# Kernel tuning notes

Measured on AMD Instinct MI355X. Metric: run time of the kernel, lower is better.

Reference implementation:

```python
import jax, jax.numpy as jnp
import numpy as np

B, S, D = 32, 512, 1024
H, HD = 16, 64          # num_heads, head_dim
K = 64                  # downsampling_k
NEG = -9e15             # -9000000000000000.0 in source


def setup_inputs() -> dict:
    key0 = jax.random.key(0)
    ks = jax.random.split(key0, 8)
    glorot = lambda k, shape, fan: jax.random.uniform(k, shape, jnp.float32,
                                                      -np.sqrt(6.0 / fan), np.sqrt(6.0 / fan))
    fan = D + H * HD  # glorot_uniform over (hidden, heads*head_dim)
    return {
        "query": jax.random.normal(ks[0], (B, S, D), jnp.float32),
        "key": jax.random.normal(ks[1], (B, S, D), jnp.float32),
        "value": jax.random.normal(ks[2], (B, S, D), jnp.float32),
        "query_kernel": glorot(ks[3], (D, H, HD), fan),
        "key_kernel": glorot(ks[4], (D, H, HD), fan),
        "value_kernel": glorot(ks[5], (D, H, HD), fan),
        "key_downsample_mat": (1.0 / K) * jax.random.normal(ks[6], (K, S), jnp.float32),
        "value_downsample_mat": (1.0 / K) * jax.random.normal(ks[7], (K, S), jnp.float32),
    }


def reference(query, key, value, query_kernel, key_kernel, value_kernel,
              key_downsample_mat, value_downsample_mat):
    # Linformer-style downsampling of K/V along the sequence axis: [B,S,D] -> [B,K,D]
    key_ds = jnp.einsum('ks,bsd->bkd', key_downsample_mat, key)
    val_ds = jnp.einsum('ks,bsd->bkd', value_downsample_mat, value)

    # Per-head projections
    q = jnp.einsum('bsd,dnh->bsnh', query, query_kernel)   # [B,S,H,HD]
    k = jnp.einsum('bkd,dnh->bknh', key_ds, key_kernel)    # [B,K,H,HD]
    v = jnp.einsum('bkd,dnh->bknh', val_ds, value_kernel)  # [B,K,H,HD]

    # Masked softmax attention over the downsampled key set
    scores = jnp.einsum('bqnh,bknh->bnqk', q, k)           # [B,H,S,K]
    # Source builds tril over [S, K_down] then slices first K cols (no-op here)
    mask = jnp.tril(jnp.ones((S, K), dtype=bool))          # [S,K], broadcasts over B,H
    scores = jnp.where(mask, scores, NEG)
    attn = jax.nn.softmax(scores, axis=-1)                 # dropout deterministic (train=False)

    a_v = jnp.einsum('bnqk,bknh->bqnh', attn, v)           # [B,S,H,HD]
    return a_v.reshape(B, S, H * HD)
```

## Files before the change

kernel.cpp:

```cpp
#include <hip/hip_runtime.h>
#include <stdint.h>

#define B_   32
#define S_   512
#define D_   1024
#define H_   16
#define HD_  64
#define KD_  64
#define NH_  1024

typedef __attribute__((ext_vector_type(8))) short short8;
typedef __attribute__((ext_vector_type(4))) float floatx4;

#define GAS __attribute__((address_space(1)))
#define LAS __attribute__((address_space(3)))

__device__ __forceinline__ ushort f2bf(float f) {
  uint32_t u = __float_as_uint(f);
  u = u + 0x7FFFu + ((u >> 16) & 1u);
  return (ushort)(u >> 16);
}

__device__ __forceinline__ float bf2f(ushort h) {
  return __uint_as_float(((uint32_t)h) << 16);
}

__device__ __forceinline__ void gload_lds16(const void* g, void* l) {
  __builtin_amdgcn_global_load_lds((const GAS uint32_t*)g, (LAS uint32_t*)l, 16, 0, 0);
}

#define BARRIER() asm volatile("s_barrier" ::: "memory")
#define WAITLGKM() asm volatile("s_waitcnt lgkmcnt(0)" ::: "memory")

__global__ __launch_bounds__(256) void cvt_split(const float* __restrict__ kdm,
                                                 const float* __restrict__ vdm,
                                                 ushort* __restrict__ hi,
                                                 ushort* __restrict__ lo) {
  int i = blockIdx.x * 256 + threadIdx.x;
  const float* src = (i < 8192) ? kdm : vdm;
  int j = i & 8191;
  float4 v = ((const float4*)src)[j];
  ushort4 h, l;
  h.x = f2bf(v.x); l.x = f2bf(v.x - bf2f(h.x));
  h.y = f2bf(v.y); l.y = f2bf(v.y - bf2f(h.y));
  h.z = f2bf(v.z); l.z = f2bf(v.z - bf2f(h.z));
  h.w = f2bf(v.w); l.w = f2bf(v.w - bf2f(h.w));
  ((ushort4*)hi)[i] = h;
  ((ushort4*)lo)[i] = l;
}

__global__ __launch_bounds__(256, 6) void fused_pre(
    const float* __restrict__ query, const float* __restrict__ key,
    const float* __restrict__ value, const float* __restrict__ qk,
    const float* __restrict__ kkm, const float* __restrict__ vkm,
    const ushort* __restrict__ dsm_hi, const ushort* __restrict__ dsm_lo,
    ushort* __restrict__ q_bf, ushort* __restrict__ qkT,
    ushort* __restrict__ kkT, ushort* __restrict__ vkT,
    ushort* __restrict__ outk, ushort* __restrict__ outv) {
  __shared__ __align__(16) char smem[26624];
  const int blk = blockIdx.x;
  const int tid = threadIdx.x;

  if (blk < 512) {
    const int bz = (blk & 7) + ((blk >> 6) << 3);
    const int t  = (blk >> 3) & 7;
    const int z = bz >> 5, b = bz & 31;
    const int c0 = t * 128;
    const float* in = z ? value : key;
    ushort* out     = z ? outv : outk;
    const ushort* Ah = dsm_hi + (size_t)z * (KD_ * S_);
    const ushort* Al = dsm_lo + (size_t)z * (KD_ * S_);

    ushort* lAh = (ushort*)smem;
    ushort* lAl = (ushort*)(smem + 4096);
    uint*   lBh = (uint*)(smem + 8192);
    uint*   lBl = (uint*)(smem + 17408);

    const int lane = tid & 63, w = tid >> 6;
    const int lr = lane & 15, lg = lane >> 4;
    const int wn = w * 32;
    const int lam = tid & 31;
    const int d0 = lam * 4;
    const int sp = tid >> 5;

    floatx4 acc[4][2];
#pragma unroll
    for (int m = 0; m < 4; ++m)
#pragma unroll
      for (int n = 0; n < 2; ++n) acc[m][n] = (floatx4){0.f, 0.f, 0.f, 0.f};

    for (int k0 = 0; k0 < S_; k0 += 32) {
      {
        size_t src = (size_t)(tid >> 2) * S_ + k0 + (size_t)(tid & 3) * 8;
        gload_lds16(Ah + src, lAh + w * 512);
        gload_lds16(Al + src, lAl + w * 512);
      }
      float4 ra[2], rb[2];
#pragma unroll
      for (int si = 0; si < 2; ++si) {
        int s = sp * 2 + si * 16;
        const float* p = in + ((size_t)(b * S_ + k0 + s)) * D_ + c0 + d0;
        ra[si] = *(const float4*)p;
        rb[si] = *(const float4*)(p + D_);
      }
      const int swz = lam & 12;
#pragma unroll
      for (int si = 0; si < 2; ++si) {
        int col = (sp + si * 8) ^ swz;
        const float* pa = (const float*)&ra[si];
        const float* pb = (const float*)&rb[si];
#pragma unroll
        for (int i = 0; i < 4; ++i) {
          ushort h0 = f2bf(pa[i]);
          ushort l0 = f2bf(pa[i] - bf2f(h0));
          ushort h1 = f2bf(pb[i]);
          ushort l1 = f2bf(pb[i] - bf2f(h1));
          lBh[(d0 + i) * 18 + col] = (uint)h0 | ((uint)h1 << 16);
          lBl[(d0 + i) * 18 + col] = (uint)l0 | ((uint)l1 << 16);
        }
      }
      __syncthreads();
      short8 bh[2], bl[2];
#pragma unroll
      for (int n = 0; n < 2; ++n) {
        int d = wn + n * 16 + lr;
        int off = d * 18 + ((lg * 4) ^ ((d >> 2) & 12));
        bh[n] = *(const short8*)&lBh[off];
        bl[n] = *(const short8*)&lBl[off];
      }
#pragma unroll
      for (int m = 0; m < 4; ++m) {
        int aoff = (m * 16 + lr) * 32 + lg * 8;
        short8 ah = *(const short8*)&lAh[aoff];
        short8 al = *(const short8*)&lAl[aoff];
#pragma unroll
        for (int n = 0; n < 2; ++n) {
          acc[m][n] = __builtin_amdgcn_mfma_f32_16x16x32_bf16(ah, bh[n], acc[m][n], 0, 0, 0);
          acc[m][n] = __builtin_amdgcn_mfma_f32_16x16x32_bf16(ah, bl[n], acc[m][n], 0, 0, 0);
          acc[m][n] = __builtin_amdgcn_mfma_f32_16x16x32_bf16(al, bh[n], acc[m][n], 0, 0, 0);
        }
      }
      __syncthreads();
    }
    size_t obase = (size_t)b * KD_ * D_;
#pragma unroll
    for (int m = 0; m < 4; ++m)
#pragma unroll
      for (int n = 0; n < 2; ++n)
#pragma unroll
        for (int r = 0; r < 4; ++r)
          out[obase + (size_t)(m * 16 + lg * 4 + r) * D_ + c0 + wn + n * 16 + lr] =
              f2bf(acc[m][n][r]);

  } else if (blk < 512 + 3072) {
    const int blk2 = blk - 512;
    const int tz = blk2 >> 10;
    const int rem = blk2 & 1023;
    const int tyb = rem >> 5;
    const int txb = rem & 31;
    const float* in = tz == 0 ? qk : (tz == 1 ? kkm : vkm);
    ushort* outp    = tz == 0 ? qkT : (tz == 1 ? kkT : vkT);
    float (*tile)[33] = (float(*)[33])smem;
    const int tx = tid & 31, ty = tid >> 5;
    int x = txb * 32 + tx;
    int y0 = tyb * 32;
#pragma unroll
    for (int j = 0; j < 4; ++j)
      tile[ty + j * 8][tx] = in[(size_t)(y0 + ty + j * 8) * 1024 + x];
    __syncthreads();
    int x2 = tyb * 32 + tx;
    int y2 = txb * 32;
#pragma unroll
    for (int j = 0; j < 4; ++j)
      outp[(size_t)(y2 + ty + j * 8) * 1024 + x2] = f2bf(tile[tx][ty + j * 8]);

  } else {
    const size_t base = (size_t)(blk - 3584) * 2048 + tid;
#pragma unroll
    for (int j = 0; j < 8; ++j) {
      size_t i = base + (size_t)j * 256;
      float4 v = ((const float4*)query)[i];
      ushort4 o;
      o.x = f2bf(v.x); o.y = f2bf(v.y); o.z = f2bf(v.z); o.w = f2bf(v.w);
      ((ushort4*)q_bf)[i] = o;
    }
  }
}

__global__ __launch_bounds__(256) void gemm_bf16(const ushort* __restrict__ A,
                                                 const ushort* __restrict__ Bt,
                                                 const ushort* __restrict__ Bt2,
                                                 ushort* __restrict__ C,
                                                 int Kred, int MT, int mtSplit) {
  int h = blockIdx.x;
  int xcd = h & 7, slot = h >> 3;
  int mt = xcd * (MT >> 3) + (slot >> 3);
  int nt = slot & 7;
  int m0 = mt * 128, n0 = nt * 128;
  const ushort* Bsel = (mt >= mtSplit) ? Bt2 : Bt;

  __shared__ __align__(16) ushort lA[128 * 32];
  __shared__ __align__(16) ushort lB[128 * 32];
  int tid = threadIdx.x;
  int lane = tid & 63, w = tid >> 6;
  int lr = lane & 15, lg = lane >> 4;
  int wm = (w >> 1) * 64, wn = (w & 1) * 64;
  floatx4 acc[4][4];
#pragma unroll
  for (int m = 0; m < 4; ++m)
#pragma unroll
    for (int n = 0; n < 4; ++n) acc[m][n] = (floatx4){0.f, 0.f, 0.f, 0.f};

  for (int k0 = 0; k0 < Kred; k0 += 32) {
#pragma unroll
    for (int i = 0; i < 2; ++i) {
      int c = i * 256 + w * 64 + lane;
      gload_lds16(A + ((size_t)(m0 + (c >> 2)) * Kred + k0 + (c & 3) * 8),
                  &lA[(i * 256 + w * 64) * 8]);
      gload_lds16(Bsel + ((size_t)(n0 + (c >> 2)) * 1024 + k0 + (c & 3) * 8),
                  &lB[(i * 256 + w * 64) * 8]);
    }
    __syncthreads();
    short8 af[4], bf[4];
#pragma unroll
    for (int m = 0; m < 4; ++m)
      af[m] = *(const short8*)&lA[(wm + m * 16 + lr) * 32 + lg * 8];
#pragma unroll
    for (int n = 0; n < 4; ++n)
      bf[n] = *(const short8*)&lB[(wn + n * 16 + lr) * 32 + lg * 8];
#pragma unroll
    for (int m = 0; m < 4; ++m)
#pragma unroll
      for (int n = 0; n < 4; ++n)
        acc[m][n] = __builtin_amdgcn_mfma_f32_16x16x32_bf16(af[m], bf[n], acc[m][n], 0, 0, 0);
    __syncthreads();
  }
#pragma unroll
  for (int m = 0; m < 4; ++m)
#pragma unroll
    for (int n = 0; n < 4; ++n)
#pragma unroll
      for (int r = 0; r < 4; ++r)
        C[(size_t)(m0 + wm + m * 16 + lg * 4 + r) * 1024 + n0 + wn + n * 16 + lr] =
            f2bf(acc[m][n][r]);
}

__global__ __launch_bounds__(512, 2) void gemm256_attn(
    const ushort* __restrict__ A, const ushort* __restrict__ Bt,
    const ushort* __restrict__ kp, const ushort* __restrict__ vp,
    float* __restrict__ out) {
  extern __shared__ ushort lds[];
  ushort* ldsA = lds;
  ushort* ldsB = lds + 2 * 256 * 64;
  const int tid = threadIdx.x;
  const int w = tid >> 6, lane = tid & 63;
  const int lr = lane & 15, lg = lane >> 4;
  const int wm = w >> 2, wn = w & 3;
  const int bid = blockIdx.x;
  const int mt = (bid & 7) * 8 + ((bid >> 3) >> 2);
  const int nt = (bid >> 3) & 3;
  const int m0 = mt * 256, n0 = nt * 256;
  const int NT = 16;

  const int srow = tid >> 3;
  const int sslot = tid & 7;

  auto stageA = [&](int sl, int ch, int k0) {
    int rloc = ch * 64 + srow;
    int gs = sslot ^ (rloc & 7);
    gload_lds16(A + (size_t)(m0 + rloc) * 1024 + k0 + gs * 8,
                ldsA + sl * (256 * 64) + ch * (64 * 64) + w * 512);
  };
  auto stageB = [&](int sl, int ch, int k0) {
    int rloc = ch * 64 + srow;
    int gs = sslot ^ (rloc & 7);
    gload_lds16(Bt + (size_t)(n0 + rloc) * 1024 + k0 + gs * 8,
                ldsB + sl * (256 * 64) + ch * (64 * 64) + w * 512);
  };

  short8 af[4][2], bf[2][2];
  auto loadA = [&](int sl, int mh) {
#pragma unroll
    for (int i = 0; i < 4; ++i) {
      int row = wm * 128 + (mh * 4 + i) * 16 + lr;
#pragma unroll
      for (int kk = 0; kk < 2; ++kk) {
        int col = (((kk * 4 + lg) ^ (row & 7)) * 8);
        af[i][kk] = *(const short8*)&ldsA[sl * (256 * 64) + row * 64 + col];
      }
    }
  };
  auto loadB = [&](int sl, int nh) {
#pragma unroll
    for (int j = 0; j < 2; ++j) {
      int row = wn * 64 + (nh * 2 + j) * 16 + lr;
#pragma unroll
      for (int kk = 0; kk < 2; ++kk) {
        int col = (((kk * 4 + lg) ^ (row & 7)) * 8);
        bf[j][kk] = *(const short8*)&ldsB[sl * (256 * 64) + row * 64 + col];
      }
    }
  };

  floatx4 acc[8][4];
#pragma unroll
  for (int i = 0; i < 8; ++i)
#pragma unroll
    for (int j = 0; j < 4; ++j) acc[i][j] = (floatx4){0.f, 0.f, 0.f, 0.f};

  auto mma16 = [&](int mh, int nh) {
    __builtin_amdgcn_s_setprio(1);
#pragma unroll
    for (int i = 0; i < 4; ++i)
#pragma unroll
      for (int j = 0; j < 2; ++j)
#pragma unroll
        for (int kk = 0; kk < 2; ++kk)
          acc[mh * 4 + i][nh * 2 + j] = __builtin_amdgcn_mfma_f32_16x16x32_bf16(
              af[i][kk], bf[j][kk], acc[mh * 4 + i][nh * 2 + j], 0, 0, 0);
    __builtin_amdgcn_s_setprio(0);
  };

#pragma unroll
  for (int ch = 0; ch < 4; ++ch) { stageA(0, ch, 0); stageB(0, ch, 0); }

#pragma unroll 2
  for (int t = 0; t < NT; ++t) {
    const int s = t & 1, ns = s ^ 1;
    const int kn = (t + 1) << 6;
    const bool more = (t + 1 < NT);
    if (more) { stageA(ns, 0, kn); stageA(ns, 1, kn); }
    if (more) { asm volatile("s_waitcnt vmcnt(2)" ::: "memory"); }
    else      { asm volatile("s_waitcnt vmcnt(0)" ::: "memory"); }
    BARRIER();
    loadA(s, 0); loadB(s, 0);
    WAITLGKM();
    mma16(0, 0);
    BARRIER();
    loadB(s, 1);
    if (more) { stageB(ns, 0, kn); stageB(ns, 1, kn); }
    BARRIER();
    WAITLGKM();
    mma16(0, 1);
    BARRIER();
    loadA(s, 1);
    if (more) { stageA(ns, 2, kn); stageA(ns, 3, kn); }
    BARRIER();
    WAITLGKM();
    mma16(1, 1);
    BARRIER();
    loadB(s, 0);
    if (more) { stageB(ns, 2, kn); stageB(ns, 3, kn); }
    BARRIER();
    WAITLGKM();
    mma16(1, 0);
    BARRIER();
  }

  ushort* QP = lds + w * 4608;
  ushort* sV = lds + 8 * 4608;
  const int b = mt >> 1;
  const int hq = nt * 4 + wn;

  {
    int hh = tid >> 7, t2 = tid & 127;
    int k = t2 >> 1, h0 = (t2 & 1) * 32;
    const ushort* src = vp + ((size_t)b * KD_ + k) * 1024 + (nt * 4 + hh) * HD_ + h0;
#pragma unroll
    for (int i = 0; i < 32; ++i) sV[hh * 4608 + (h0 + i) * 72 + k] = src[i];
  }
  __syncthreads();

#pragma unroll
  for (int half = 0; half < 2; ++half) {
    const int srow0 = (mt & 1) * 256 + wm * 128 + half * 64;
#pragma unroll
    for (int mi = 0; mi < 4; ++mi)
#pragma unroll
      for (int nj = 0; nj < 4; ++nj)
#pragma unroll
        for (int r = 0; r < 4; ++r)
          QP[(mi * 16 + lg * 4 + r) * 72 + nj * 16 + lr] =
              f2bf(acc[half * 4 + mi][nj][r]);
    WAITLGKM();
    __builtin_amdgcn_sched_barrier(0);
    floatx4 qacc[4][4];
#pragma unroll
    for (int m = 0; m < 4; ++m)
#pragma unroll
      for (int n = 0; n < 4; ++n) qacc[m][n] = (floatx4){0.f, 0.f, 0.f, 0.f};
#pragma unroll
    for (int kk = 0; kk < 2; ++kk) {
      short8 qa[4], kb[4];
#pragma unroll
      for (int m = 0; m < 4; ++m)
        qa[m] = *(const short8*)&QP[(m * 16 + lr) * 72 + kk * 32 + lg * 8];
#pragma unroll
      for (int n = 0; n < 4; ++n)
        kb[n] = *(const short8*)(kp + ((size_t)b * KD_ + n * 16 + lr) * 1024 +
                                 hq * HD_ + kk * 32 + lg * 8);
#pragma unroll
      for (int m = 0; m < 4; ++m)
#pragma unroll
        for (int n = 0; n < 4; ++n)
          qacc[m][n] = __builtin_amdgcn_mfma_f32_16x16x32_bf16(qa[m], kb[n], qacc[m][n], 0, 0, 0);
    }
#pragma unroll
    for (int m = 0; m < 4; ++m) {
#pragma unroll
      for (int r = 0; r < 4; ++r) {
        int srow2 = srow0 + m * 16 + lg * 4 + r;
        float vals[4];
        float mx = -1e30f;
#pragma unroll
        for (int n = 0; n < 4; ++n) {
          int col = n * 16 + lr;
          float val = qacc[m][n][r];
          val = (col <= srow2) ? val : -1e30f;
          vals[n] = val;
          mx = fmaxf(mx, val);
        }
        mx = fmaxf(mx, __shfl_xor(mx, 1));
        mx = fmaxf(mx, __shfl_xor(mx, 2));
        mx = fmaxf(mx, __shfl_xor(mx, 4));
        mx = fmaxf(mx, __shfl_xor(mx, 8));
        float sum = 0.f;
#pragma unroll
        for (int n = 0; n < 4; ++n) {
          float e = __expf(vals[n] - mx);
          vals[n] = e;
          sum += e;
        }
        sum += __shfl_xor(sum, 1);
        sum += __shfl_xor(sum, 2);
        sum += __shfl_xor(sum, 4);
        sum += __shfl_xor(sum, 8);
        float inv = 1.0f / sum;
#pragma unroll
        for (int n = 0; n < 4; ++n)
          QP[(m * 16 + lg * 4 + r) * 72 + n * 16 + lr] = f2bf(vals[n] * inv);
      }
    }
    WAITLGKM();
    __builtin_amdgcn_sched_barrier(0);
    floatx4 oacc[4][4];
#pragma unroll
    for (int m = 0; m < 4; ++m)
#pragma unroll
      for (int n = 0; n < 4; ++n) oacc[m][n] = (floatx4){0.f, 0.f, 0.f, 0.f};
#pragma unroll
    for (int kk = 0; kk < 2; ++kk) {
      short8 pa[4], vb[4];
#pragma unroll
      for (int m = 0; m < 4; ++m)
        pa[m] = *(const short8*)&QP[(m * 16 + lr) * 72 + kk * 32 + lg * 8];
#pragma unroll
      for (int n = 0; n < 4; ++n)
        vb[n] = *(const short8*)&sV[wn * 4608 + (n * 16 + lr) * 72 + kk * 32 + lg * 8];
#pragma unroll
      for (int m = 0; m < 4; ++m)
#pragma unroll
        for (int n = 0; n < 4; ++n)
          oacc[m][n] = __builtin_amdgcn_mfma_f32_16x16x32_bf16(pa[m], vb[n], oacc[m][n], 0, 0, 0);
    }
#pragma unroll
    for (int m = 0; m < 4; ++m)
#pragma unroll
      for (int n = 0; n < 4; ++n)
#pragma unroll
        for (int r = 0; r < 4; ++r)
          out[((size_t)b * S_ + srow0 + m * 16 + lg * 4 + r) * 1024 +
              hq * HD_ + n * 16 + lr] = oacc[m][n][r];
  }
}

extern "C" void kernel_launch(void* const* d_in, const int* in_sizes, int n_in,
                              void* d_out, int out_size, void* d_ws, size_t ws_size,
                              hipStream_t stream) {
  const float* query = (const float*)d_in[0];
  const float* key   = (const float*)d_in[1];
  const float* value = (const float*)d_in[2];
  const float* qk    = (const float*)d_in[3];
  const float* kk    = (const float*)d_in[4];
  const float* vk    = (const float*)d_in[5];
  const float* kdm   = (const float*)d_in[6];
  const float* vdm   = (const float*)d_in[7];
  float* out = (float*)d_out;

  char* ws = (char*)d_ws;
  if (ws_size < (90ull << 20)) return;
  ushort* q_bf   = (ushort*)(ws);
  ushort* qkT    = (ushort*)(ws + (33ull << 20));
  ushort* kkT    = (ushort*)(ws + (35ull << 20));
  ushort* vkT    = (ushort*)(ws + (37ull << 20));
  ushort* kds    = (ushort*)(ws + (39ull << 20));
  ushort* vds    = (ushort*)(ws + (43ull << 20));
  ushort* k_proj = (ushort*)(ws + (79ull << 20));
  ushort* v_proj = (ushort*)(ws + (83ull << 20));
  ushort* dsm_hi = (ushort*)(ws + (87ull << 20));
  ushort* dsm_lo = (ushort*)(ws + (87ull << 20) + (128ull << 10));

  hipFuncSetAttribute((const void*)gemm256_attn,
                      hipFuncAttributeMaxDynamicSharedMemorySize, 131072);

  cvt_split<<<64, 256, 0, stream>>>(kdm, vdm, dsm_hi, dsm_lo);
  fused_pre<<<512 + 3072 + 2048, 256, 0, stream>>>(
      query, key, value, qk, kk, vk, dsm_hi, dsm_lo,
      q_bf, qkT, kkT, vkT, kds, vds);
  gemm_bf16<<<256, 256, 0, stream>>>(kds, kkT, vkT, k_proj, 1024, 32, 16);
  gemm256_attn<<<256, 512, 131072, stream>>>(q_bf, qkT, k_proj, v_proj, out);
}
```

Baseline: 134.3 us.

## Move query cast and query-kernel transpose into the K/V projection GEMM launch

The query-kernel transpose and the query fp32-to-bf16 cast move out of the preprocessing kernel and into the K/V projection GEMM launch as extra independent blocks. The preprocessing kernel then only handles the K/V downsampling and the K/V kernel transposes. This shortens the critical-path preprocessing launch and lets the bandwidth-bound query conversion overlap the compute-bound projection GEMM. The GEMM blocks are dispatched first, so the extra blocks fill idle CUs, but they may compete with the GEMM for memory bandwidth and add block-index branching.

```diff
diff --git a/kernel.cpp b/kernel.cpp
--- a/kernel.cpp
+++ b/kernel.cpp
@@ -49,12 +49,10 @@
   ((ushort4*)lo)[i] = l;
 }
 
-__global__ __launch_bounds__(256, 6) void fused_pre(
-    const float* __restrict__ query, const float* __restrict__ key,
-    const float* __restrict__ value, const float* __restrict__ qk,
+__global__ __launch_bounds__(256, 6) void pre_kv(
+    const float* __restrict__ key, const float* __restrict__ value,
     const float* __restrict__ kkm, const float* __restrict__ vkm,
     const ushort* __restrict__ dsm_hi, const ushort* __restrict__ dsm_lo,
-    ushort* __restrict__ q_bf, ushort* __restrict__ qkT,
     ushort* __restrict__ kkT, ushort* __restrict__ vkT,
     ushort* __restrict__ outk, ushort* __restrict__ outv) {
   __shared__ __align__(16) char smem[26624];
@@ -152,14 +150,14 @@
           out[obase + (size_t)(m * 16 + lg * 4 + r) * D_ + c0 + wn + n * 16 + lr] =
               f2bf(acc[m][n][r]);
 
-  } else if (blk < 512 + 3072) {
+  } else {
     const int blk2 = blk - 512;
     const int tz = blk2 >> 10;
     const int rem = blk2 & 1023;
     const int tyb = rem >> 5;
     const int txb = rem & 31;
-    const float* in = tz == 0 ? qk : (tz == 1 ? kkm : vkm);
-    ushort* outp    = tz == 0 ? qkT : (tz == 1 ? kkT : vkT);
+    const float* in = tz == 0 ? kkm : vkm;
+    ushort* outp    = tz == 0 ? kkT : vkT;
     float (*tile)[33] = (float(*)[33])smem;
     const int tx = tid & 31, ty = tid >> 5;
     int x = txb * 32 + tx;
@@ -173,9 +171,91 @@
 #pragma unroll
     for (int j = 0; j < 4; ++j)
       outp[(size_t)(y2 + ty + j * 8) * 1024 + x2] = f2bf(tile[tx][ty + j * 8]);
+  }
+}
+
+__global__ __launch_bounds__(256) void gemm_kv_q(
+    const ushort* __restrict__ A,
+    const ushort* __restrict__ Bt,
+    const ushort* __restrict__ Bt2,
+    ushort* __restrict__ C,
+    const float* __restrict__ qk, ushort* __restrict__ qkT,
+    const float* __restrict__ query, ushort* __restrict__ q_bf) {
+  __shared__ __align__(16) char smem[16384];
+  const int blk = blockIdx.x;
+  const int tid = threadIdx.x;
+
+  if (blk < 256) {
+    ushort* lA = (ushort*)smem;
+    ushort* lB = (ushort*)(smem + 8192);
+    int xcd = blk & 7, slot = blk >> 3;
+    int mt = xcd * 4 + (slot >> 3);
+    int nt = slot & 7;
+    int m0 = mt * 128, n0 = nt * 128;
+    const ushort* Bsel = (mt >= 16) ? Bt2 : Bt;
+
+    int lane = tid & 63, w = tid >> 6;
+    int lr = lane & 15, lg = lane >> 4;
+    int wm = (w >> 1) * 64, wn = (w & 1) * 64;
+    floatx4 acc[4][4];
+#pragma unroll
+    for (int m = 0; m < 4; ++m)
+#pragma unroll
+      for (int n = 0; n < 4; ++n) acc[m][n] = (floatx4){0.f, 0.f, 0.f, 0.f};
+
+    for (int k0 = 0; k0 < 1024; k0 += 32) {
+#pragma unroll
+      for (int i = 0; i < 2; ++i) {
+        int c = i * 256 + w * 64 + lane;
+        gload_lds16(A + ((size_t)(m0 + (c >> 2)) * 1024 + k0 + (c & 3) * 8),
+                    &lA[(i * 256 + w * 64) * 8]);
+        gload_lds16(Bsel + ((size_t)(n0 + (c >> 2)) * 1024 + k0 + (c & 3) * 8),
+                    &lB[(i * 256 + w * 64) * 8]);
+      }
+      __syncthreads();
+      short8 af[4], bfr[4];
+#pragma unroll
+      for (int m = 0; m < 4; ++m)
+        af[m] = *(const short8*)&lA[(wm + m * 16 + lr) * 32 + lg * 8];
+#pragma unroll
+      for (int n = 0; n < 4; ++n)
+        bfr[n] = *(const short8*)&lB[(wn + n * 16 + lr) * 32 + lg * 8];
+#pragma unroll
+      for (int m = 0; m < 4; ++m)
+#pragma unroll
+        for (int n = 0; n < 4; ++n)
+          acc[m][n] = __builtin_amdgcn_mfma_f32_16x16x32_bf16(af[m], bfr[n], acc[m][n], 0, 0, 0);
+      __syncthreads();
+    }
+#pragma unroll
+    for (int m = 0; m < 4; ++m)
+#pragma unroll
+      for (int n = 0; n < 4; ++n)
+#pragma unroll
+        for (int r = 0; r < 4; ++r)
+          C[(size_t)(m0 + wm + m * 16 + lg * 4 + r) * 1024 + n0 + wn + n * 16 + lr] =
+              f2bf(acc[m][n][r]);
+
+  } else if (blk < 256 + 1024) {
+    const int blk2 = blk - 256;
+    const int tyb = blk2 >> 5;
+    const int txb = blk2 & 31;
+    float (*tile)[33] = (float(*)[33])smem;
+    const int tx = tid & 31, ty = tid >> 5;
+    int x = txb * 32 + tx;
+    int y0 = tyb * 32;
+#pragma unroll
+    for (int j = 0; j < 4; ++j)
+      tile[ty + j * 8][tx] = qk[(size_t)(y0 + ty + j * 8) * 1024 + x];
+    __syncthreads();
+    int x2 = tyb * 32 + tx;
+    int y2 = txb * 32;
+#pragma unroll
+    for (int j = 0; j < 4; ++j)
+      qkT[(size_t)(y2 + ty + j * 8) * 1024 + x2] = f2bf(tile[tx][ty + j * 8]);
 
   } else {
-    const size_t base = (size_t)(blk - 3584) * 2048 + tid;
+    const size_t base = (size_t)(blk - 1280) * 2048 + tid;
 #pragma unroll
     for (int j = 0; j < 8; ++j) {
       size_t i = base + (size_t)j * 256;
@@ -185,64 +265,6 @@
       ((ushort4*)q_bf)[i] = o;
     }
   }
-}
-
-__global__ __launch_bounds__(256) void gemm_bf16(const ushort* __restrict__ A,
-                                                 const ushort* __restrict__ Bt,
-                                                 const ushort* __restrict__ Bt2,
-                                                 ushort* __restrict__ C,
-                                                 int Kred, int MT, int mtSplit) {
-  int h = blockIdx.x;
-  int xcd = h & 7, slot = h >> 3;
-  int mt = xcd * (MT >> 3) + (slot >> 3);
-  int nt = slot & 7;
-  int m0 = mt * 128, n0 = nt * 128;
-  const ushort* Bsel = (mt >= mtSplit) ? Bt2 : Bt;
-
-  __shared__ __align__(16) ushort lA[128 * 32];
-  __shared__ __align__(16) ushort lB[128 * 32];
-  int tid = threadIdx.x;
-  int lane = tid & 63, w = tid >> 6;
-  int lr = lane & 15, lg = lane >> 4;
-  int wm = (w >> 1) * 64, wn = (w & 1) * 64;
-  floatx4 acc[4][4];
-#pragma unroll
-  for (int m = 0; m < 4; ++m)
-#pragma unroll
-    for (int n = 0; n < 4; ++n) acc[m][n] = (floatx4){0.f, 0.f, 0.f, 0.f};
-
-  for (int k0 = 0; k0 < Kred; k0 += 32) {
-#pragma unroll
-    for (int i = 0; i < 2; ++i) {
-      int c = i * 256 + w * 64 + lane;
-      gload_lds16(A + ((size_t)(m0 + (c >> 2)) * Kred + k0 + (c & 3) * 8),
-                  &lA[(i * 256 + w * 64) * 8]);
-      gload_lds16(Bsel + ((size_t)(n0 + (c >> 2)) * 1024 + k0 + (c & 3) * 8),
-                  &lB[(i * 256 + w * 64) * 8]);
-    }
-    __syncthreads();
-    short8 af[4], bf[4];
-#pragma unroll
-    for (int m = 0; m < 4; ++m)
-      af[m] = *(const short8*)&lA[(wm + m * 16 + lr) * 32 + lg * 8];
-#pragma unroll
-    for (int n = 0; n < 4; ++n)
-      bf[n] = *(const short8*)&lB[(wn + n * 16 + lr) * 32 + lg * 8];
-#pragma unroll
-    for (int m = 0; m < 4; ++m)
-#pragma unroll
-      for (int n = 0; n < 4; ++n)
-        acc[m][n] = __builtin_amdgcn_mfma_f32_16x16x32_bf16(af[m], bf[n], acc[m][n], 0, 0, 0);
-    __syncthreads();
-  }
-#pragma unroll
-  for (int m = 0; m < 4; ++m)
-#pragma unroll
-    for (int n = 0; n < 4; ++n)
-#pragma unroll
-      for (int r = 0; r < 4; ++r)
-        C[(size_t)(m0 + wm + m * 16 + lg * 4 + r) * 1024 + n0 + wn + n * 16 + lr] =
-            f2bf(acc[m][n][r]);
 }
 
 __global__ __launch_bounds__(512, 2) void gemm256_attn(
@@ -504,9 +526,9 @@
                       hipFuncAttributeMaxDynamicSharedMemorySize, 131072);
 
   cvt_split<<<64, 256, 0, stream>>>(kdm, vdm, dsm_hi, dsm_lo);
-  fused_pre<<<512 + 3072 + 2048, 256, 0, stream>>>(
-      query, key, value, qk, kk, vk, dsm_hi, dsm_lo,
-      q_bf, qkT, kkT, vkT, kds, vds);
-  gemm_bf16<<<256, 256, 0, stream>>>(kds, kkT, vkT, k_proj, 1024, 32, 16);
+  pre_kv<<<512 + 2048, 256, 0, stream>>>(
+      key, value, kk, vk, dsm_hi, dsm_lo, kkT, vkT, kds, vds);
+  gemm_kv_q<<<256 + 1024 + 2048, 256, 0, stream>>>(
+      kds, kkT, vkT, k_proj, qk, qkT, query, q_bf);
   gemm256_attn<<<256, 512, 131072, stream>>>(q_bf, qkT, k_proj, v_proj, out);
 }
```

Result: faster. 129.6 us (-3.5%).
